# Optimization experiments

Measured on AMD Instinct MI355X. Metric: run time of the kernel, lower is better.

The kernel has to match this reference:

```python
import jax, jax.numpy as jnp
import numpy as np

NEG_INF = -1e9  # large negative instead of -inf for safe masked softmax
LRELU_ALPHA = 0.2


def setup_inputs() -> dict:
    key = jax.random.key(0)
    k1, k2, k3, k4, k5 = jax.random.split(key, 5)
    B, N, Din, H, F = 8, 1024, 256, 4, 64
    X = jax.random.normal(k1, (B, N, Din), dtype=jnp.float32)
    A = jax.random.randint(k2, (B, N, N), 0, 2).astype(jnp.int32)
    # xavier-ish scaled params
    W = jax.random.normal(k3, (Din, H * F), dtype=jnp.float32) * np.sqrt(2.0 / (Din + H * F))
    a_src = jax.random.normal(k4, (H, F), dtype=jnp.float32) * np.sqrt(2.0 / (1 + F))
    a_dst = jax.random.normal(k5, (H, F), dtype=jnp.float32) * np.sqrt(2.0 / (1 + F))
    return {"X": X, "A": A, "W": W, "a_src": a_src, "a_dst": a_dst}


def reference(X, A, W, a_src, a_dst):
    B, N, _ = X.shape
    H, F = a_src.shape
    Wh = (X @ W).reshape(B, N, H, F)                       # [B,N,H,F]
    e_src = jnp.einsum('bnhf,hf->bnh', Wh, a_src)          # [B,N,H]
    e_dst = jnp.einsum('bjhf,hf->bjh', Wh, a_dst)          # [B,N,H]
    # additive scores: e[b,i,j,h] = lrelu(e_src[b,i,h] + e_dst[b,j,h])
    e = jax.nn.leaky_relu(e_src[:, :, None, :] + e_dst[:, None, :, :], LRELU_ALPHA)
    mask = (A > 0)[..., None]                              # [B,N,N,1]
    e = jnp.where(mask, e, NEG_INF)
    alpha = jax.nn.softmax(e, axis=2)                      # softmax over source j
    # dropout is identity in eval mode
    Hout = jnp.einsum('bijh,bjhf->bihf', alpha, Wh)        # [B,N,H,F]
    Hout = jax.nn.elu(Hout)
    return Hout.reshape(B, N, H * F)
```

## Files before the change

kernel.cpp:

```cpp
#include <hip/hip_runtime.h>


typedef unsigned short u16;
typedef short bf16x8 __attribute__((ext_vector_type(8)));
typedef unsigned short u16x8 __attribute__((ext_vector_type(8)));
typedef float f32x4 __attribute__((ext_vector_type(4)));

__device__ __forceinline__ u16 f2bf(float f) {
  unsigned u = __float_as_uint(f);
  unsigned r = (u + 0x7FFFu + ((u >> 16) & 1u)) >> 16;
  return (u16)r;
}
__device__ __forceinline__ float bf2f(u16 h) {
  return __uint_as_float(((unsigned)h) << 16);
}

__device__ __forceinline__ bool detect_bf16(const void* p) {
  const u16* u = (const u16*)p;
  u16 v = u[2 * (threadIdx.x & 63)];
  int ex = (v >> 7) & 0xFF;
  unsigned long long b = __ballot(ex >= 112 && ex <= 142);
  return __popcll(b) >= 48;
}

__global__ __launch_bounds__(256) void prep_kernel(
    const void* __restrict__ X, const int* __restrict__ A,
    const void* __restrict__ W, const void* __restrict__ asrc,
    const void* __restrict__ adst,
    u16* __restrict__ xhi, u16* __restrict__ xlo,
    u16* __restrict__ wthi, u16* __restrict__ wtlo,
    float* __restrict__ aF, unsigned long long* __restrict__ Apack, int use_lo) {
  const int bid = blockIdx.x, t = threadIdx.x;
  if (bid < 1024) {
    const bool bf = detect_bf16(X);
    const int i0 = (bid * 256 + t) * 8;
    float v[8];
    if (bf) {
      u16x8 raw = *(const u16x8*)((const u16*)X + i0);
#pragma unroll
      for (int j = 0; j < 8; ++j) v[j] = bf2f((u16)raw[j]);
    } else {
      const float* Xf = (const float*)X;
#pragma unroll
      for (int j = 0; j < 8; ++j) v[j] = Xf[i0 + j];
    }
    u16x8 hi, lo;
#pragma unroll
    for (int j = 0; j < 8; ++j) {
      u16 h = f2bf(v[j]);
      hi[j] = h;
      lo[j] = f2bf(v[j] - bf2f(h));
    }
    *(u16x8*)(xhi + i0) = hi;
    if (use_lo) *(u16x8*)(xlo + i0) = lo;
  } else if (bid < 1282) {
    const bool bf = detect_bf16(X);
    const int wb = bid - 1024;
    if (wb < 256) {
      const int n = wb, k = t;
      float v = bf ? bf2f(((const u16*)W)[k * 256 + n]) : ((const float*)W)[k * 256 + n];
      u16 h = f2bf(v);
      wthi[n * 256 + k] = h;
      if (use_lo) wtlo[n * 256 + k] = f2bf(v - bf2f(h));
    } else if (wb == 256) {
      aF[t] = bf ? bf2f(((const u16*)asrc)[t]) : ((const float*)asrc)[t];
    } else {
      aF[256 + t] = bf ? bf2f(((const u16*)adst)[t]) : ((const float*)adst)[t];
    }
  } else {
    const int wid = ((bid - 1282) * 256 + t) >> 6;
    const int l = t & 63;
#pragma unroll
    for (int g = 0; g < 16; ++g) {
      const long base = ((long)(wid * 16 + g)) << 6;
      int a = A[base + l];
      unsigned long long m = __ballot(a > 0);
      if (l == 0) Apack[wid * 16 + g] = m;
    }
  }
}

__global__ __launch_bounds__(256) void gemm_kernel(
    const u16* __restrict__ Xhi, const u16* __restrict__ Xlo,
    const u16* __restrict__ WThi, const u16* __restrict__ WTlo,
    const float* __restrict__ aF,
    u16* __restrict__ WhThi,
    float* __restrict__ esT, float* __restrict__ edT, int use_lo) {
  __shared__ __align__(16) u16 As[64 * 32];
  __shared__ __align__(16) u16 Bs[64 * 32];
  __shared__ __align__(16) u16 Asl[64 * 32];
  __shared__ __align__(16) u16 Bsl[64 * 32];
  const int sbid = (blockIdx.x & 7) * 64 + (blockIdx.x >> 3);
  const int bm = sbid >> 2, h = sbid & 3;
  const int t = threadIdx.x, w = t >> 6, l = t & 63;
  const int sr = t >> 2, sc = (t & 3) * 8;
  const int lm = l & 15, lk = (l >> 4) * 8;
  f32x4 acc[4] = {{0,0,0,0},{0,0,0,0},{0,0,0,0},{0,0,0,0}};
  const int xrow = (bm * 64 + sr) * 256 + sc;
  const int wrow = (h * 64 + sr) * 256 + sc;
  for (int k0 = 0; k0 < 256; k0 += 32) {
    __syncthreads();
    *(u16x8*)&As[sr * 32 + sc] = *(const u16x8*)&Xhi[xrow + k0];
    *(u16x8*)&Bs[sr * 32 + sc] = *(const u16x8*)&WThi[wrow + k0];
    if (use_lo) {
      *(u16x8*)&Asl[sr * 32 + sc] = *(const u16x8*)&Xlo[xrow + k0];
      *(u16x8*)&Bsl[sr * 32 + sc] = *(const u16x8*)&WTlo[wrow + k0];
    }
    __syncthreads();
    bf16x8 af = *(const bf16x8*)&As[(w * 16 + lm) * 32 + lk];
#pragma unroll
    for (int ns = 0; ns < 4; ++ns) {
      bf16x8 bfr = *(const bf16x8*)&Bs[(ns * 16 + lm) * 32 + lk];
      acc[ns] = __builtin_amdgcn_mfma_f32_16x16x32_bf16(af, bfr, acc[ns], 0, 0, 0);
      if (use_lo) {
        bf16x8 afl = *(const bf16x8*)&Asl[(w * 16 + lm) * 32 + lk];
        bf16x8 bfl = *(const bf16x8*)&Bsl[(ns * 16 + lm) * 32 + lk];
        acc[ns] = __builtin_amdgcn_mfma_f32_16x16x32_bf16(afl, bfr, acc[ns], 0, 0, 0);
        acc[ns] = __builtin_amdgcn_mfma_f32_16x16x32_bf16(af, bfl, acc[ns], 0, 0, 0);
      }
    }
  }
  float asv[4], adv[4];
#pragma unroll
  for (int ns = 0; ns < 4; ++ns) {
    asv[ns] = aF[h * 64 + ns * 16 + lm];
    adv[ns] = aF[256 + h * 64 + ns * 16 + lm];
  }
#pragma unroll
  for (int j = 0; j < 4; ++j) {
    const int m = bm * 64 + w * 16 + (l >> 4) * 4 + j;
    const int bi = m >> 10, jr = m & 1023;
    float psrc = 0.f, pdst = 0.f;
#pragma unroll
    for (int ns = 0; ns < 4; ++ns) {
      float v = acc[ns][j];
      WhThi[((bi * 4 + h) * 64 + ns * 16 + lm) * 1024 + jr] = f2bf(v);
      psrc += v * asv[ns];
      pdst += v * adv[ns];
    }
#pragma unroll
    for (int mm = 1; mm < 16; mm <<= 1) {
      psrc += __shfl_xor(psrc, mm);
      pdst += __shfl_xor(pdst, mm);
    }
    if (lm == 0) {
      esT[(bi * 4 + h) * 1024 + jr] = psrc;
      edT[(bi * 4 + h) * 1024 + jr] = pdst;
    }
  }
}

__global__ __launch_bounds__(1024, 4) void attn_kernel(
    const void* __restrict__ Xraw, const unsigned* __restrict__ Apack,
    const u16* __restrict__ WhThi,
    const float* __restrict__ esT, const float* __restrict__ edT,
    void* __restrict__ out) {
  __shared__ __align__(16) u16 Vs[2][2][8192];
  __shared__ __align__(16) float eds[2][2][128];
  __shared__ float combL[8][64][17];
  __shared__ float dsumc[8][16];
  const bool outbf = detect_bf16(Xraw);
  const int t = threadIdx.x, l = t & 63, w = t >> 6;
  const int rg = w & 7, half = w >> 3;
  const int sbid = (blockIdx.x & 7) * 32 + (blockIdx.x >> 3);
  const int h = sbid & 3, it = (sbid >> 2) & 7, b = sbid >> 5;
  const int i0 = it * 128, bh = b * 4 + h;
  const int lm = l & 15, lkg = l >> 4;
  const int row = i0 + rg * 16 + lm;
  const float esl = esT[bh * 1024 + row];
  const float* edp = edT + bh * 1024;
  const u16* whbase = WhThi + (size_t)bh * 65536;
  const uint4* amp = (const uint4*)Apack + (size_t)(b * 1024 + row) * 8 + half * 4;

  const int f0 = t >> 4, s0 = t & 15;
  const int wr0 = (f0 * 16 + (s0 ^ (f0 & 7))) * 8;
  const u16* gp = whbase + f0 * 1024 + s0 * 8;
  const int ehalf = (t >> 6) & 1;

  f32x4 acc[4] = {{0,0,0,0},{0,0,0,0},{0,0,0,0},{0,0,0,0}};
  float dsum = 0.f;
  const int swz = (lm & 7) << 3;

  uint4 cm = amp[0];
  {
    *(bf16x8*)&Vs[0][0][wr0] = *(const bf16x8*)(gp);
    *(bf16x8*)&Vs[0][1][wr0] = *(const bf16x8*)(gp + 512);
    if (t < 128) *(float2*)&eds[0][ehalf][(t & 63) * 2] =
        *(const float2*)(edp + ehalf * 512 + (t & 63) * 2);
  }
  __syncthreads();

#pragma unroll
  for (int jt = 0; jt < 4; ++jt) {
    const int cur = jt & 1;
    bf16x8 na = {}, nb = {};
    float2 ne = {};
    uint4 nm = {};
    if (jt < 3) {
      na = *(const bf16x8*)(gp + (jt + 1) * 128);
      nb = *(const bf16x8*)(gp + 512 + (jt + 1) * 128);
      if (t < 128) ne = *(const float2*)(edp + ehalf * 512 + (jt + 1) * 128 + (t & 63) * 2);
      nm = amp[jt + 1];
    }
#pragma unroll
    for (int ks = 0; ks < 4; ++ks) {
      const unsigned mword = (ks == 0) ? cm.x : (ks == 1) ? cm.y
                           : (ks == 2) ? cm.z : cm.w;
      const unsigned mb = mword >> (lkg * 8);
      float4 e0 = *(const float4*)&eds[cur][half][ks * 32 + lkg * 8];
      float4 e1 = *(const float4*)&eds[cur][half][ks * 32 + lkg * 8 + 4];
      const float ed8[8] = {e0.x, e0.y, e0.z, e0.w, e1.x, e1.y, e1.z, e1.w};
      float p[8];
#pragma unroll
      for (int jj = 0; jj < 8; ++jj) {
        float scv = esl + ed8[jj];
        scv = fmaxf(scv, 0.2f * scv);
        p[jj] = ((mb >> jj) & 1u) ? __expf(scv) : 0.f;
        dsum += p[jj];
      }
      union { unsigned u[4]; bf16x8 v; } afu;
#pragma unroll
      for (int q = 0; q < 4; ++q)
        asm("v_cvt_pk_bf16_f32 %0, %1, %2" : "=v"(afu.u[q]) : "v"(p[2*q]), "v"(p[2*q+1]));
      const int jb = (ks * 32 + lkg * 8) ^ swz;
#pragma unroll
      for (int ns = 0; ns < 4; ++ns) {
        bf16x8 vf = *(const bf16x8*)&Vs[cur][half][(ns * 16 + lm) * 128 + jb];
        acc[ns] = __builtin_amdgcn_mfma_f32_16x16x32_bf16(afu.v, vf, acc[ns], 0, 0, 0);
      }
    }
    if (jt < 3) {
      *(bf16x8*)&Vs[cur ^ 1][0][wr0] = na;
      *(bf16x8*)&Vs[cur ^ 1][1][wr0] = nb;
      if (t < 128) *(float2*)&eds[cur ^ 1][ehalf][(t & 63) * 2] = ne;
      cm = nm;
    }
    __syncthreads();
  }

  dsum += __shfl_xor(dsum, 16);
  dsum += __shfl_xor(dsum, 32);

  if (half == 1) {
#pragma unroll
    for (int ns = 0; ns < 4; ++ns)
#pragma unroll
      for (int j = 0; j < 4; ++j) combL[rg][l][ns * 4 + j] = acc[ns][j];
    if (l < 16) dsumc[rg][l] = dsum;
  }
  __syncthreads();
  if (half == 0) {
#pragma unroll
    for (int j = 0; j < 4; ++j) {
      const int irow = (l >> 4) * 4 + j;
      const float den = __shfl(dsum, irow) + dsumc[rg][irow];
      const float rinv = den > 0.f ? 1.0f / den : 0.f;
      const int rowoff = (b * 1024 + i0 + rg * 16 + irow) * 256 + h * 64;
#pragma unroll
      for (int ns = 0; ns < 4; ++ns) {
        float v = (acc[ns][j] + combL[rg][l][ns * 4 + j]) * rinv;
        v = v > 0.f ? v : (__expf(v) - 1.0f);
        const int off = rowoff + ns * 16 + lm;
        if (outbf) ((u16*)out)[off] = f2bf(v);
        else       ((float*)out)[off] = v;
      }
    }
  }
}

extern "C" void kernel_launch(void* const* d_in, const int* in_sizes, int n_in,
                              void* d_out, int out_size, void* d_ws, size_t ws_size,
                              hipStream_t stream) {
  const void* X = d_in[0];
  const int* A = (const int*)d_in[1];
  const void* W = d_in[2];
  const void* asrc = d_in[3];
  const void* adst = d_in[4];

  char* ws = (char*)d_ws;
  size_t off = 0;
  auto alloc = [&](size_t bytes) -> void* {
    void* p = ws + off;
    off += (bytes + 255) & ~(size_t)255;
    return p;
  };
  u16* Xhi = (u16*)alloc((size_t)2097152 * 2);
  u16* WhThi = (u16*)alloc((size_t)2097152 * 2);
  u16* WThi = (u16*)alloc((size_t)65536 * 2);
  float* esT = (float*)alloc((size_t)32768 * 4);
  float* edT = (float*)alloc((size_t)32768 * 4);
  float* aF = (float*)alloc((size_t)512 * 4);
  unsigned long long* Apack = (unsigned long long*)alloc((size_t)131072 * 8);
  const size_t base_need = off;
  if (ws_size < base_need) return;

  int use_lo = 0;
  u16 *Xlo = Xhi, *WTlo = WThi;
  const size_t lo_extra = (size_t)2097152 * 2 + 65536 * 2 + 512;
  if (ws_size >= base_need + lo_extra) {
    use_lo = 1;
    Xlo = (u16*)alloc((size_t)2097152 * 2);
    WTlo = (u16*)alloc((size_t)65536 * 2);
  }

  prep_kernel<<<3330, 256, 0, stream>>>(X, A, W, asrc, adst, Xhi, Xlo, WThi, WTlo, aF, Apack, use_lo);
  gemm_kernel<<<512, 256, 0, stream>>>(Xhi, Xlo, WThi, WTlo, aF, WhThi, esT, edT, use_lo);
  attn_kernel<<<256, 1024, 0, stream>>>(X, (const unsigned*)Apack, WhThi, esT, edT, d_out);
}
```

Baseline: 51.19 us.

## Drop bf16 hi/lo split GEMM and split attention into partial and combine kernels

```diff
diff --git a/kernel.cpp b/kernel.cpp
--- a/kernel.cpp
+++ b/kernel.cpp
@@ -27,41 +27,28 @@
     const void* __restrict__ X, const int* __restrict__ A,
     const void* __restrict__ W, const void* __restrict__ asrc,
     const void* __restrict__ adst,
-    u16* __restrict__ xhi, u16* __restrict__ xlo,
-    u16* __restrict__ wthi, u16* __restrict__ wtlo,
-    float* __restrict__ aF, unsigned long long* __restrict__ Apack, int use_lo) {
+    u16* __restrict__ xhi, u16* __restrict__ wthi,
+    float* __restrict__ aF, unsigned long long* __restrict__ Apack) {
   const int bid = blockIdx.x, t = threadIdx.x;
   if (bid < 1024) {
     const bool bf = detect_bf16(X);
     const int i0 = (bid * 256 + t) * 8;
-    float v[8];
+    u16x8 hi;
     if (bf) {
-      u16x8 raw = *(const u16x8*)((const u16*)X + i0);
-#pragma unroll
-      for (int j = 0; j < 8; ++j) v[j] = bf2f((u16)raw[j]);
+      hi = *(const u16x8*)((const u16*)X + i0);
     } else {
       const float* Xf = (const float*)X;
 #pragma unroll
-      for (int j = 0; j < 8; ++j) v[j] = Xf[i0 + j];
-    }
-    u16x8 hi, lo;
-#pragma unroll
-    for (int j = 0; j < 8; ++j) {
-      u16 h = f2bf(v[j]);
-      hi[j] = h;
-      lo[j] = f2bf(v[j] - bf2f(h));
+      for (int j = 0; j < 8; ++j) hi[j] = f2bf(Xf[i0 + j]);
     }
     *(u16x8*)(xhi + i0) = hi;
-    if (use_lo) *(u16x8*)(xlo + i0) = lo;
   } else if (bid < 1282) {
     const bool bf = detect_bf16(X);
     const int wb = bid - 1024;
     if (wb < 256) {
       const int n = wb, k = t;
       float v = bf ? bf2f(((const u16*)W)[k * 256 + n]) : ((const float*)W)[k * 256 + n];
-      u16 h = f2bf(v);
-      wthi[n * 256 + k] = h;
-      if (use_lo) wtlo[n * 256 + k] = f2bf(v - bf2f(h));
+      wthi[n * 256 + k] = f2bf(v);
     } else if (wb == 256) {
       aF[t] = bf ? bf2f(((const u16*)asrc)[t]) : ((const float*)asrc)[t];
     } else {
@@ -81,15 +68,12 @@
 }
 
 __global__ __launch_bounds__(256) void gemm_kernel(
-    const u16* __restrict__ Xhi, const u16* __restrict__ Xlo,
-    const u16* __restrict__ WThi, const u16* __restrict__ WTlo,
+    const u16* __restrict__ Xhi, const u16* __restrict__ WThi,
     const float* __restrict__ aF,
     u16* __restrict__ WhThi,
-    float* __restrict__ esT, float* __restrict__ edT, int use_lo) {
+    float* __restrict__ esT, float* __restrict__ edT) {
   __shared__ __align__(16) u16 As[64 * 32];
   __shared__ __align__(16) u16 Bs[64 * 32];
-  __shared__ __align__(16) u16 Asl[64 * 32];
-  __shared__ __align__(16) u16 Bsl[64 * 32];
   const int sbid = (blockIdx.x & 7) * 64 + (blockIdx.x >> 3);
   const int bm = sbid >> 2, h = sbid & 3;
   const int t = threadIdx.x, w = t >> 6, l = t & 63;
@@ -102,22 +86,12 @@
     __syncthreads();
     *(u16x8*)&As[sr * 32 + sc] = *(const u16x8*)&Xhi[xrow + k0];
     *(u16x8*)&Bs[sr * 32 + sc] = *(const u16x8*)&WThi[wrow + k0];
-    if (use_lo) {
-      *(u16x8*)&Asl[sr * 32 + sc] = *(const u16x8*)&Xlo[xrow + k0];
-      *(u16x8*)&Bsl[sr * 32 + sc] = *(const u16x8*)&WTlo[wrow + k0];
-    }
     __syncthreads();
     bf16x8 af = *(const bf16x8*)&As[(w * 16 + lm) * 32 + lk];
 #pragma unroll
     for (int ns = 0; ns < 4; ++ns) {
       bf16x8 bfr = *(const bf16x8*)&Bs[(ns * 16 + lm) * 32 + lk];
       acc[ns] = __builtin_amdgcn_mfma_f32_16x16x32_bf16(af, bfr, acc[ns], 0, 0, 0);
-      if (use_lo) {
-        bf16x8 afl = *(const bf16x8*)&Asl[(w * 16 + lm) * 32 + lk];
-        bf16x8 bfl = *(const bf16x8*)&Bsl[(ns * 16 + lm) * 32 + lk];
-        acc[ns] = __builtin_amdgcn_mfma_f32_16x16x32_bf16(afl, bfr, acc[ns], 0, 0, 0);
-        acc[ns] = __builtin_amdgcn_mfma_f32_16x16x32_bf16(af, bfl, acc[ns], 0, 0, 0);
-      }
     }
   }
   float asv[4], adv[4];
@@ -146,6 +120,129 @@
     if (lm == 0) {
       esT[(bi * 4 + h) * 1024 + jr] = psrc;
       edT[(bi * 4 + h) * 1024 + jr] = pdst;
+    }
+  }
+}
+
+__global__ __launch_bounds__(512, 4) void attn_part_kernel(
+    const unsigned* __restrict__ Apack, const u16* __restrict__ WhThi,
+    const float* __restrict__ esT, const float* __restrict__ edT,
+    float* __restrict__ accP, float* __restrict__ dsumP) {
+  __shared__ __align__(16) u16 Vs[2][8192];
+  __shared__ __align__(16) float eds[2][128];
+  const int t = threadIdx.x, l = t & 63, w = t >> 6;
+  const int sbid = (blockIdx.x & 7) * 64 + (blockIdx.x >> 3);
+  const int half = sbid & 1, h = (sbid >> 1) & 3, it = (sbid >> 3) & 7, b = sbid >> 6;
+  const int i0 = it * 128, bh = b * 4 + h;
+  const int lm = l & 15, lkg = l >> 4;
+  const int row = i0 + w * 16 + lm;
+  const float esl = esT[bh * 1024 + row];
+  const float* edp = edT + bh * 1024 + half * 512;
+  const u16* whbase = WhThi + (size_t)bh * 65536 + half * 512;
+  const uint4* amp = (const uint4*)Apack + (size_t)(b * 1024 + row) * 8 + half * 4;
+
+  const int f0 = t >> 4, s0 = t & 15;
+  const int f1 = (t + 512) >> 4;
+  const int wr0 = (f0 * 16 + (s0 ^ (f0 & 7))) * 8;
+  const int wr1 = (f1 * 16 + (s0 ^ (f1 & 7))) * 8;
+  const u16* g0p = whbase + f0 * 1024 + s0 * 8;
+  const u16* g1p = whbase + f1 * 1024 + s0 * 8;
+
+  f32x4 acc[4] = {{0,0,0,0},{0,0,0,0},{0,0,0,0},{0,0,0,0}};
+  float dsum = 0.f;
+  const int swz = (lm & 7) << 3;
+
+  uint4 cm = amp[0];
+  {
+    *(bf16x8*)&Vs[0][wr0] = *(const bf16x8*)(g0p);
+    *(bf16x8*)&Vs[0][wr1] = *(const bf16x8*)(g1p);
+    if (t < 64) *(float2*)&eds[0][t * 2] = *(const float2*)(edp + t * 2);
+  }
+  __syncthreads();
+
+#pragma unroll
+  for (int jt = 0; jt < 4; ++jt) {
+    const int cur = jt & 1;
+    bf16x8 na = {}, nb = {};
+    float2 ne = {};
+    uint4 nm = {};
+    if (jt < 3) {
+      na = *(const bf16x8*)(g0p + (jt + 1) * 128);
+      nb = *(const bf16x8*)(g1p + (jt + 1) * 128);
+      if (t < 64) ne = *(const float2*)(edp + (jt + 1) * 128 + t * 2);
+      nm = amp[jt + 1];
+    }
+#pragma unroll
+    for (int ks = 0; ks < 4; ++ks) {
+      const unsigned mword = (ks == 0) ? cm.x : (ks == 1) ? cm.y
+                           : (ks == 2) ? cm.z : cm.w;
+      const unsigned mb = mword >> (lkg * 8);
+      float4 e0 = *(const float4*)&eds[cur][ks * 32 + lkg * 8];
+      float4 e1 = *(const float4*)&eds[cur][ks * 32 + lkg * 8 + 4];
+      const float ed8[8] = {e0.x, e0.y, e0.z, e0.w, e1.x, e1.y, e1.z, e1.w};
+      float p[8];
+#pragma unroll
+      for (int jj = 0; jj < 8; ++jj) {
+        float scv = esl + ed8[jj];
+        scv = fmaxf(scv, 0.2f * scv);
+        p[jj] = ((mb >> jj) & 1u) ? __expf(scv) : 0.f;
+        dsum += p[jj];
+      }
+      union { unsigned u[4]; bf16x8 v; } afu;
+#pragma unroll
+      for (int q = 0; q < 4; ++q)
+        asm("v_cvt_pk_bf16_f32 %0, %1, %2" : "=v"(afu.u[q]) : "v"(p[2*q]), "v"(p[2*q+1]));
+      const int jb = (ks * 32 + lkg * 8) ^ swz;
+#pragma unroll
+      for (int ns = 0; ns < 4; ++ns) {
+        bf16x8 vf = *(const bf16x8*)&Vs[cur][(ns * 16 + lm) * 128 + jb];
+        acc[ns] = __builtin_amdgcn_mfma_f32_16x16x32_bf16(afu.v, vf, acc[ns], 0, 0, 0);
+      }
+    }
+    if (jt < 3) {
+      *(bf16x8*)&Vs[cur ^ 1][wr0] = na;
+      *(bf16x8*)&Vs[cur ^ 1][wr1] = nb;
+      if (t < 64) *(float2*)&eds[cur ^ 1][t * 2] = ne;
+      cm = nm;
+    }
+    __syncthreads();
+  }
+
+  dsum += __shfl_xor(dsum, 16);
+  dsum += __shfl_xor(dsum, 32);
+
+  f32x4* ap4 = (f32x4*)accP;
+#pragma unroll
+  for (int ns = 0; ns < 4; ++ns)
+    ap4[((size_t)sbid * 4 + ns) * 512 + t] = acc[ns];
+  if (l < 16) dsumP[(sbid * 8 + w) * 16 + l] = dsum;
+}
+
+__global__ __launch_bounds__(512) void attn_comb_kernel(
+    const void* __restrict__ Xraw, const float* __restrict__ accP,
+    const float* __restrict__ dsumP, void* __restrict__ out) {
+  const bool outbf = detect_bf16(Xraw);
+  const int t = threadIdx.x, l = t & 63, w = t >> 6;
+  const int c = (blockIdx.x & 7) * 32 + (blockIdx.x >> 3);
+  const int h = c & 3, it = (c >> 2) & 7, b = c >> 5;
+  const int sA = ((b * 8 + it) * 4 + h) * 2;
+  const int sB = sA + 1;
+  const int i0 = it * 128, lm = l & 15;
+  const f32x4* ap4 = (const f32x4*)accP;
+#pragma unroll
+  for (int ns = 0; ns < 4; ++ns) {
+    f32x4 a4 = ap4[((size_t)sA * 4 + ns) * 512 + t];
+    f32x4 b4 = ap4[((size_t)sB * 4 + ns) * 512 + t];
+#pragma unroll
+    for (int j = 0; j < 4; ++j) {
+      const int irow = (l >> 4) * 4 + j;
+      const float den = dsumP[(sA * 8 + w) * 16 + irow] + dsumP[(sB * 8 + w) * 16 + irow];
+      const float rinv = den > 0.f ? 1.0f / den : 0.f;
+      float v = (a4[j] + b4[j]) * rinv;
+      v = v > 0.f ? v : (__expf(v) - 1.0f);
+      const int off = (b * 1024 + i0 + w * 16 + irow) * 256 + h * 64 + ns * 16 + lm;
+      if (outbf) ((u16*)out)[off] = f2bf(v);
+      else       ((float*)out)[off] = v;
     }
   }
 }
@@ -294,16 +391,24 @@
   const size_t base_need = off;
   if (ws_size < base_need) return;
 
-  int use_lo = 0;
-  u16 *Xlo = Xhi, *WTlo = WThi;
-  const size_t lo_extra = (size_t)2097152 * 2 + 65536 * 2 + 512;
-  if (ws_size >= base_need + lo_extra) {
-    use_lo = 1;
-    Xlo = (u16*)alloc((size_t)2097152 * 2);
-    WTlo = (u16*)alloc((size_t)65536 * 2);
-  }
-
-  prep_kernel<<<3330, 256, 0, stream>>>(X, A, W, asrc, adst, Xhi, Xlo, WThi, WTlo, aF, Apack, use_lo);
-  gemm_kernel<<<512, 256, 0, stream>>>(Xhi, Xlo, WThi, WTlo, aF, WhThi, esT, edT, use_lo);
-  attn_kernel<<<256, 1024, 0, stream>>>(X, (const unsigned*)Apack, WhThi, esT, edT, d_out);
-}
+  float* accP = nullptr;
+  float* dsumP = nullptr;
+  int use_split = 0;
+  {
+    const size_t need_split = base_need + ((size_t)16777216 + 256) + ((size_t)262144 + 256);
+    if (ws_size >= need_split) {
+      use_split = 1;
+      accP = (float*)alloc((size_t)16777216);
+      dsumP = (float*)alloc((size_t)262144);
+    }
+  }
+
+  prep_kernel<<<3330, 256, 0, stream>>>(X, A, W, asrc, adst, Xhi, WThi, aF, Apack);
+  gemm_kernel<<<512, 256, 0, stream>>>(Xhi, WThi, aF, WhThi, esT, edT);
+  if (use_split) {
+    attn_part_kernel<<<512, 512, 0, stream>>>((const unsigned*)Apack, WhThi, esT, edT, accP, dsumP);
+    attn_comb_kernel<<<256, 512, 0, stream>>>(X, accP, dsumP, d_out);
+  } else {
+    attn_kernel<<<256, 1024, 0, stream>>>(X, (const unsigned*)Apack, WhThi, esT, edT, d_out);
+  }
+}
```

Result: faster. 49.66 us (-3.0%).
